# Kernel optimization log

Hardware: AMD Instinct MI355X
Metric: run time of the kernel (lower is better)

The kernel has to match this reference:

```python
import jax, jax.numpy as jnp
import numpy as np

B, D, C, K = 1024, 64, 100000, 5  # batch, feature dim, n_classes, positives per sample


def setup_inputs() -> dict:
    key = jax.random.key(0)
    k1, k2, k3 = jax.random.split(key, 3)
    x = jax.random.normal(k1, (B, D), dtype=jnp.float32)
    W = jax.random.normal(k2, (D, C), dtype=jnp.float32) * 0.02
    b = jnp.zeros((C,), dtype=jnp.float32)
    # K distinct positive class ids per sample (setdiff1d assume_unique requires distinct)
    base = jax.random.randint(k3, (B, 1), 0, C)
    labels = (base + jnp.arange(K, dtype=jnp.int64)[None, :]) % C
    return {"x": x, "labels": labels, "W": W, "b": b}


def reference(x, labels, W, b):
    # classifier: logits [B, C]
    logits = x @ W + b
    # Original loop: for each positive p of a sample, CE over [p] + negatives
    # (negatives = all classes except ALL positives of that sample), label 0:
    #   loss_p = -(l_p - log(exp(l_p) + sum_{c in negatives} exp(l_c)))
    # Vectorized via total expsum minus the positives' contribution.
    m = jnp.max(logits, axis=1, keepdims=True)                    # [B, 1]
    e = jnp.exp(logits - m)                                       # [B, C]
    total = jnp.sum(e, axis=1, keepdims=True)                     # [B, 1]
    pos_logits = jnp.take_along_axis(logits, labels, axis=1)      # [B, K]
    pos_e = jnp.exp(pos_logits - m)                               # [B, K]
    neg_sum = total - jnp.sum(pos_e, axis=1, keepdims=True)       # [B, 1]
    denom = pos_e + neg_sum                                       # [B, K]
    losses = -(pos_logits - m - jnp.log(denom))                   # [B, K]
    # sum over all (sample, positive) pairs / total number of positives
    return jnp.sum(losses) / losses.size
```

## Files before the change

kernel.cpp:

```cpp
#include <hip/hip_runtime.h>

constexpr int Bn = 1024;
constexpr int Dn = 64;
constexpr int Cn = 100000;
constexpr int Kn = 5;
constexpr float LOG2E = 1.44269504088896f;

typedef float f32x4  __attribute__((ext_vector_type(4)));
typedef short bf16x8 __attribute__((ext_vector_type(8)));

__device__ __forceinline__ unsigned short f32_to_bf16(float f) {
  union { float f; unsigned int u; } v; v.f = f;
  unsigned int r = v.u + 0x7FFFu + ((v.u >> 16) & 1u);
  return (unsigned short)(r >> 16);
}
__device__ __forceinline__ float bf16_to_f32(unsigned short u) {
  union { unsigned int i; float f; } v; v.i = ((unsigned int)u) << 16; return v.f;
}

constexpr int SPLITS = 125;
constexpr int CPS    = Cn / SPLITS;
constexpr int NCH    = CPS / 32;
constexpr int SGRPS  = 4;
constexpr int NBLK_W = (Cn + 63) / 64;
constexpr int GEMM_GRID = 512;

__global__ __launch_bounds__(256) void prep_kernel(
    const float* __restrict__ x, const float* __restrict__ W,
    unsigned short* __restrict__ xb, unsigned short* __restrict__ Wt,
    float* __restrict__ out)
{
  const int tid = threadIdx.x;
  const int b   = blockIdx.x;
  if (b == 0 && tid == 0) *out = 0.f;
  if (b < NBLK_W) {
    __shared__ unsigned short tile[64][71];
    const int c0   = b * 64;
    const int cIdx = tid & 63, dIdx = tid >> 6;
#pragma unroll
    for (int k = 0; k < 16; ++k) {
      const int d = dIdx * 16 + k;
      const int c = c0 + cIdx;
      const float v = (c < Cn) ? W[(size_t)d * Cn + c] : 0.f;
      tile[d][cIdx] = f32_to_bf16(v);
    }
    __syncthreads();
    const int cl = tid >> 2, dq = tid & 3;
    if (c0 + cl < Cn) {
      bf16x8 o0, o1;
#pragma unroll
      for (int k = 0; k < 8; ++k) o0[k] = (short)tile[dq * 16 + k][cl];
#pragma unroll
      for (int k = 0; k < 8; ++k) o1[k] = (short)tile[dq * 16 + 8 + k][cl];
      unsigned short* dst = Wt + (size_t)(c0 + cl) * 64 + dq * 16;
      *reinterpret_cast<bf16x8*>(dst)     = o0;
      *reinterpret_cast<bf16x8*>(dst + 8) = o1;
    }
  } else {
    const int i = ((b - NBLK_W) * 256 + tid) * 4;
    if (i < Bn * Dn) {
      const float4 v = *reinterpret_cast<const float4*>(x + i);
      ushort4 o;
      o.x = f32_to_bf16(v.x); o.y = f32_to_bf16(v.y);
      o.z = f32_to_bf16(v.z); o.w = f32_to_bf16(v.w);
      *reinterpret_cast<ushort4*>(xb + i) = o;
    }
  }
}

__device__ __forceinline__ void loadChunk(
    const unsigned short* __restrict__ Wt, const float* __restrict__ bias,
    int cb, int lr, int lg, bf16x8 (&b)[2][2], float (&bb)[2])
{
  const unsigned short* p0 = Wt + (size_t)(cb + lr) * 64 + lg * 8;
  const unsigned short* p1 = p0 + 16 * 64;
  b[0][0] = *reinterpret_cast<const bf16x8*>(p0);
  b[0][1] = *reinterpret_cast<const bf16x8*>(p0 + 32);
  b[1][0] = *reinterpret_cast<const bf16x8*>(p1);
  b[1][1] = *reinterpret_cast<const bf16x8*>(p1 + 32);
  bb[0] = bias[cb + lr] * LOG2E;
  bb[1] = bias[cb + 16 + lr] * LOG2E;
}

__device__ __forceinline__ void computeChunk(
    const bf16x8 (&a)[4][2], const bf16x8 (&b)[2][2], const float (&bb)[2],
    float (&esum)[4][4])
{
  f32x4 acc[4][2];
#pragma unroll
  for (int t = 0; t < 4; ++t) {
    acc[t][0] = f32x4{0.f, 0.f, 0.f, 0.f};
    acc[t][1] = f32x4{0.f, 0.f, 0.f, 0.f};
  }
#pragma unroll
  for (int t = 0; t < 4; ++t) {
    acc[t][0] = __builtin_amdgcn_mfma_f32_16x16x32_bf16(a[t][0], b[0][0], acc[t][0], 0, 0, 0);
    acc[t][1] = __builtin_amdgcn_mfma_f32_16x16x32_bf16(a[t][0], b[1][0], acc[t][1], 0, 0, 0);
    acc[t][0] = __builtin_amdgcn_mfma_f32_16x16x32_bf16(a[t][1], b[0][1], acc[t][0], 0, 0, 0);
    acc[t][1] = __builtin_amdgcn_mfma_f32_16x16x32_bf16(a[t][1], b[1][1], acc[t][1], 0, 0, 0);
  }
#pragma unroll
  for (int t = 0; t < 4; ++t)
#pragma unroll
    for (int j = 0; j < 4; ++j) {
      const float e0 = __builtin_amdgcn_exp2f(fmaf(acc[t][0][j], LOG2E, bb[0]));
      const float e1 = __builtin_amdgcn_exp2f(fmaf(acc[t][1][j], LOG2E, bb[1]));
      esum[t][j] += e0 + e1;
    }
}

__global__ __launch_bounds__(256) void gemm_expsum_kernel(
    const unsigned short* __restrict__ xb, const unsigned short* __restrict__ Wt,
    const float* __restrict__ bias, float* __restrict__ P)
{
  const int b    = blockIdx.x;
  const int xcd  = b & 7;
  const int slot = b >> 3;
  const int split = xcd * 16 + (slot >> 2);
  const int sgrp  = slot & 3;
  if (split >= SPLITS) return;

  const int tid  = threadIdx.x;
  const int lane = tid & 63, wid = tid >> 6;
  const int lr = lane & 15, lg = lane >> 4;
  const int sbase = sgrp * 256 + wid * 64;
  const int cb0   = split * CPS;

  bf16x8 a[4][2];
#pragma unroll
  for (int t = 0; t < 4; ++t) {
    const unsigned short* ap = xb + (size_t)(sbase + t * 16 + lr) * 64 + lg * 8;
    a[t][0] = *reinterpret_cast<const bf16x8*>(ap);
    a[t][1] = *reinterpret_cast<const bf16x8*>(ap + 32);
  }

  float esum[4][4];
#pragma unroll
  for (int t = 0; t < 4; ++t)
#pragma unroll
    for (int j = 0; j < 4; ++j) esum[t][j] = 0.f;

  bf16x8 bX[2][2]; float bbX[2];
  bf16x8 bY[2][2]; float bbY[2];
  loadChunk(Wt, bias, cb0, lr, lg, bX, bbX);
#pragma unroll 1
  for (int ch = 0; ch < NCH; ch += 2) {
    if (ch + 1 < NCH) loadChunk(Wt, bias, cb0 + (ch + 1) * 32, lr, lg, bY, bbY);
    computeChunk(a, bX, bbX, esum);
    if (ch + 1 < NCH) {
      if (ch + 2 < NCH) loadChunk(Wt, bias, cb0 + (ch + 2) * 32, lr, lg, bX, bbX);
      computeChunk(a, bY, bbY, esum);
    }
  }

  float red[4][4];
#pragma unroll
  for (int t = 0; t < 4; ++t)
#pragma unroll
    for (int j = 0; j < 4; ++j) {
      float v = esum[t][j];
      v += __shfl_xor(v, 1, 64);
      v += __shfl_xor(v, 2, 64);
      v += __shfl_xor(v, 4, 64);
      v += __shfl_xor(v, 8, 64);
      red[t][j] = v;
    }
  if (lr == 0) {
#pragma unroll
    for (int t = 0; t < 4; ++t)
#pragma unroll
      for (int j = 0; j < 4; ++j)
        P[(size_t)(sbase + t * 16 + lg * 4 + j) * SPLITS + split] = red[t][j];
  }
}

__global__ __launch_bounds__(64) void loss2_kernel(
    const unsigned short* __restrict__ xb, const int* __restrict__ labels,
    const unsigned short* __restrict__ Wt, const float* __restrict__ bias,
    const float* __restrict__ P, float* __restrict__ out)
{
  const int i = blockIdx.x, lane = threadIdx.x;
  float acc = P[(size_t)i * SPLITS + lane];
  if (lane + 64 < SPLITS) acc += P[(size_t)i * SPLITS + lane + 64];
#pragma unroll
  for (int off = 32; off > 0; off >>= 1) acc += __shfl_xor(acc, off, 64);
  const float Si = acc;

  const float xv = bf16_to_f32(xb[i * Dn + lane]);
  float l[Kn];
#pragma unroll
  for (int p = 0; p < Kn; ++p) {
    const int c = labels[i * Kn + p];
    float v = xv * bf16_to_f32(Wt[(size_t)c * 64 + lane]);
#pragma unroll
    for (int off = 32; off > 0; off >>= 1) v += __shfl_xor(v, off, 64);
    l[p] = v + bias[c];
  }
  if (lane == 0) {
    float Psum = 0.f;
#pragma unroll
    for (int p = 0; p < Kn; ++p) Psum += __expf(l[p]);
    const float neg = Si - Psum;
    float lsum = 0.f;
#pragma unroll
    for (int p = 0; p < Kn; ++p)
      lsum += __logf(__expf(l[p]) + neg) - l[p];
    atomicAdd(out, lsum * (1.0f / (float)(Bn * Kn)));
  }
}

constexpr int NB  = 128;
constexpr int NPB = (Cn + NB - 1) / NB;
constexpr int NPBpad = 784;

__global__ __launch_bounds__(256) void cvt_x_kernel(
    const float* __restrict__ x, unsigned short* __restrict__ xb)
{
  const int i = (blockIdx.x * 256 + threadIdx.x) * 4;
  const float4 v = *reinterpret_cast<const float4*>(x + i);
  ushort4 o;
  o.x = f32_to_bf16(v.x); o.y = f32_to_bf16(v.y);
  o.z = f32_to_bf16(v.z); o.w = f32_to_bf16(v.w);
  *reinterpret_cast<ushort4*>(xb + i) = o;
}

__global__ __launch_bounds__(256) void expsum_mfma_kernel(
    const unsigned short* __restrict__ xb, const float* __restrict__ W,
    const float* __restrict__ bias, float* __restrict__ P,
    float* __restrict__ S, int use_partials)
{
  __shared__ float S_lds[4][Bn];
  const int tid  = threadIdx.x;
  const int lane = tid & 63, wid = tid >> 6;
  const int lg = lane >> 4, lr = lane & 15;
  const int cbase = blockIdx.x * NB + wid * 32;

  for (int i = tid; i < 4 * Bn; i += 256) (&S_lds[0][0])[i] = 0.f;

  bf16x8 bfrag[2][2];
  float  bval[2];
#pragma unroll
  for (int t = 0; t < 2; ++t) {
    const int c  = cbase + t * 16 + lr;
    const bool ok = (c < Cn);
    bval[t] = ok ? bias[c] * LOG2E : -1e38f;
#pragma unroll
    for (int h = 0; h < 2; ++h) {
      bf16x8 bf;
#pragma unroll
      for (int j = 0; j < 8; ++j) {
        const int d = h * 32 + lg * 8 + j;
        const float w = ok ? W[(size_t)d * Cn + c] : 0.f;
        bf[j] = (short)f32_to_bf16(w);
      }
      bfrag[t][h] = bf;
    }
  }
  __syncthreads();

#pragma unroll 1
  for (int ch = 0; ch < Bn / 16; ++ch) {
    const int s = ch * 16 + lr;
    const bf16x8 a0 = *reinterpret_cast<const bf16x8*>(xb + (size_t)s * Dn + lg * 8);
    const bf16x8 a1 = *reinterpret_cast<const bf16x8*>(xb + (size_t)s * Dn + 32 + lg * 8);
    f32x4 acc0 = {0.f, 0.f, 0.f, 0.f};
    f32x4 acc1 = {0.f, 0.f, 0.f, 0.f};
    acc0 = __builtin_amdgcn_mfma_f32_16x16x32_bf16(a0, bfrag[0][0], acc0, 0, 0, 0);
    acc1 = __builtin_amdgcn_mfma_f32_16x16x32_bf16(a0, bfrag[1][0], acc1, 0, 0, 0);
    acc0 = __builtin_amdgcn_mfma_f32_16x16x32_bf16(a1, bfrag[0][1], acc0, 0, 0, 0);
    acc1 = __builtin_amdgcn_mfma_f32_16x16x32_bf16(a1, bfrag[1][1], acc1, 0, 0, 0);

    float v[4];
#pragma unroll
    for (int j = 0; j < 4; ++j) {
      const float e0 = __builtin_amdgcn_exp2f(fmaf(acc0[j], LOG2E, bval[0]));
      const float e1 = __builtin_amdgcn_exp2f(fmaf(acc1[j], LOG2E, bval[1]));
      v[j] = e0 + e1;
    }
#pragma unroll
    for (int j = 0; j < 4; ++j) {
      v[j] += __shfl_xor(v[j], 1, 64);
      v[j] += __shfl_xor(v[j], 2, 64);
      v[j] += __shfl_xor(v[j], 4, 64);
      v[j] += __shfl_xor(v[j], 8, 64);
    }
    if (lr == 0) {
#pragma unroll
      for (int j = 0; j < 4; ++j)
        S_lds[wid][ch * 16 + lg * 4 + j] += v[j];
    }
  }
  __syncthreads();

  if (use_partials) {
    for (int s2 = tid; s2 < Bn; s2 += 256) {
      const float v = S_lds[0][s2] + S_lds[1][s2] + S_lds[2][s2] + S_lds[3][s2];
      P[(size_t)s2 * NPBpad + blockIdx.x] = v;
    }
  } else {
    for (int s2 = tid; s2 < Bn; s2 += 256) {
      const float v = S_lds[0][s2] + S_lds[1][s2] + S_lds[2][s2] + S_lds[3][s2];
      atomicAdd(&S[s2], v);
    }
  }
}

__global__ __launch_bounds__(64) void loss_kernel(
    const float* __restrict__ x, const int* __restrict__ labels,
    const float* __restrict__ W, const float* __restrict__ bias,
    const float* __restrict__ P, const float* __restrict__ S,
    float* __restrict__ out, int use_partials)
{
  const int i    = blockIdx.x;
  const int lane = threadIdx.x;

  float Si;
  if (use_partials) {
    float acc = 0.f;
    for (int j = lane; j < NPB; j += 64) acc += P[(size_t)i * NPBpad + j];
#pragma unroll
    for (int off = 32; off > 0; off >>= 1) acc += __shfl_xor(acc, off, 64);
    Si = acc;
  } else {
    Si = S[i];
  }

  const float xv = x[i * Dn + lane];
  float l[Kn];
#pragma unroll
  for (int p = 0; p < Kn; ++p) {
    const int c = labels[i * Kn + p];
    float v = xv * W[(size_t)lane * Cn + c];
#pragma unroll
    for (int off = 32; off > 0; off >>= 1) v += __shfl_xor(v, off, 64);
    l[p] = v + bias[c];
  }

  if (lane == 0) {
    float Psum = 0.f;
#pragma unroll
    for (int p = 0; p < Kn; ++p) Psum += __expf(l[p]);
    const float neg = Si - Psum;
    float lsum = 0.f;
#pragma unroll
    for (int p = 0; p < Kn; ++p)
      lsum += __logf(__expf(l[p]) + neg) - l[p];
    atomicAdd(out, lsum * (1.0f / (float)(Bn * Kn)));
  }
}

extern "C" void kernel_launch(void* const* d_in, const int* in_sizes, int n_in,
                              void* d_out, int out_size, void* d_ws, size_t ws_size,
                              hipStream_t stream) {
  const float* x      = (const float*)d_in[0];
  const int*   labels = (const int*)d_in[1];
  const float* W      = (const float*)d_in[2];
  const float* bias   = (const float*)d_in[3];
  float*       out    = (float*)d_out;
  char*        ws     = (char*)d_ws;

  const size_t off_xb = 0;
  const size_t off_P  = (size_t)Bn * Dn * 2;
  const size_t off_Wt = off_P + (size_t)SPLITS * Bn * 4;
  const size_t need_new = off_Wt + (size_t)Cn * Dn * 2;

  if (ws_size >= need_new) {
    unsigned short* xb = (unsigned short*)(ws + off_xb);
    float*          P  = (float*)(ws + off_P);
    unsigned short* Wt = (unsigned short*)(ws + off_Wt);
    const int prep_blocks = NBLK_W + (Bn * Dn) / (256 * 4);
    prep_kernel<<<prep_blocks, 256, 0, stream>>>(x, W, xb, Wt, out);
    gemm_expsum_kernel<<<GEMM_GRID, 256, 0, stream>>>(xb, Wt, bias, P);
    loss2_kernel<<<Bn, 64, 0, stream>>>(xb, labels, Wt, bias, P, out);
    return;
  }

  hipMemsetAsync(out, 0, sizeof(float), stream);
  float*          Sg = (float*)ws;
  unsigned short* xb = (unsigned short*)(ws + 4096);
  float*          Pp = (float*)(ws + 4096 + (size_t)Bn * Dn * 2);
  const size_t need_old = 4096 + (size_t)Bn * Dn * 2 + (size_t)Bn * NPBpad * 4;
  const int use_partials = (ws_size >= need_old) ? 1 : 0;
  if (!use_partials) hipMemsetAsync(Sg, 0, Bn * sizeof(float), stream);

  cvt_x_kernel<<<(Bn * Dn) / (256 * 4), 256, 0, stream>>>(x, xb);
  expsum_mfma_kernel<<<NPB, 256, 0, stream>>>(xb, W, bias, Pp, Sg, use_partials);
  loss_kernel<<<Bn, 64, 0, stream>>>(x, labels, W, bias, Pp, Sg, out, use_partials);
}
```

Baseline: 60.74 us.

## Fuse W transpose/convert and x conversion into the GEMM expsum kernel

Removes the separate prep kernel: each GEMM block now converts and transposes its own 800-column slice of W into bf16 in the workspace, and converts x to bf16 in registers, pre-scaled by log2e. The bias is folded into the MFMA accumulator's initial value, which drops the per-element fma before exp2. This saves one launch and one round trip of x through memory. In exchange, each of the 4 row-group blocks sharing a split redundantly converts the same W slice with strided, poorly coalesced column reads. The slice must also be written and synced before the MFMA loop can start.

```diff
diff --git a/kernel.cpp b/kernel.cpp
--- a/kernel.cpp
+++ b/kernel.cpp
@@ -5,6 +5,7 @@
 constexpr int Cn = 100000;
 constexpr int Kn = 5;
 constexpr float LOG2E = 1.44269504088896f;
+constexpr float LN2   = 0.69314718055994531f;
 
 typedef float f32x4  __attribute__((ext_vector_type(4)));
 typedef short bf16x8 __attribute__((ext_vector_type(8)));
@@ -21,52 +22,7 @@
 constexpr int SPLITS = 125;
 constexpr int CPS    = Cn / SPLITS;
 constexpr int NCH    = CPS / 32;
-constexpr int SGRPS  = 4;
-constexpr int NBLK_W = (Cn + 63) / 64;
 constexpr int GEMM_GRID = 512;
-
-__global__ __launch_bounds__(256) void prep_kernel(
-    const float* __restrict__ x, const float* __restrict__ W,
-    unsigned short* __restrict__ xb, unsigned short* __restrict__ Wt,
-    float* __restrict__ out)
-{
-  const int tid = threadIdx.x;
-  const int b   = blockIdx.x;
-  if (b == 0 && tid == 0) *out = 0.f;
-  if (b < NBLK_W) {
-    __shared__ unsigned short tile[64][71];
-    const int c0   = b * 64;
-    const int cIdx = tid & 63, dIdx = tid >> 6;
-#pragma unroll
-    for (int k = 0; k < 16; ++k) {
-      const int d = dIdx * 16 + k;
-      const int c = c0 + cIdx;
-      const float v = (c < Cn) ? W[(size_t)d * Cn + c] : 0.f;
-      tile[d][cIdx] = f32_to_bf16(v);
-    }
-    __syncthreads();
-    const int cl = tid >> 2, dq = tid & 3;
-    if (c0 + cl < Cn) {
-      bf16x8 o0, o1;
-#pragma unroll
-      for (int k = 0; k < 8; ++k) o0[k] = (short)tile[dq * 16 + k][cl];
-#pragma unroll
-      for (int k = 0; k < 8; ++k) o1[k] = (short)tile[dq * 16 + 8 + k][cl];
-      unsigned short* dst = Wt + (size_t)(c0 + cl) * 64 + dq * 16;
-      *reinterpret_cast<bf16x8*>(dst)     = o0;
-      *reinterpret_cast<bf16x8*>(dst + 8) = o1;
-    }
-  } else {
-    const int i = ((b - NBLK_W) * 256 + tid) * 4;
-    if (i < Bn * Dn) {
-      const float4 v = *reinterpret_cast<const float4*>(x + i);
-      ushort4 o;
-      o.x = f32_to_bf16(v.x); o.y = f32_to_bf16(v.y);
-      o.z = f32_to_bf16(v.z); o.w = f32_to_bf16(v.w);
-      *reinterpret_cast<ushort4*>(xb + i) = o;
-    }
-  }
-}
 
 __device__ __forceinline__ void loadChunk(
     const unsigned short* __restrict__ Wt, const float* __restrict__ bias,
@@ -89,8 +45,8 @@
   f32x4 acc[4][2];
 #pragma unroll
   for (int t = 0; t < 4; ++t) {
-    acc[t][0] = f32x4{0.f, 0.f, 0.f, 0.f};
-    acc[t][1] = f32x4{0.f, 0.f, 0.f, 0.f};
+    acc[t][0] = f32x4{bb[0], bb[0], bb[0], bb[0]};
+    acc[t][1] = f32x4{bb[1], bb[1], bb[1], bb[1]};
   }
 #pragma unroll
   for (int t = 0; t < 4; ++t) {
@@ -103,15 +59,16 @@
   for (int t = 0; t < 4; ++t)
 #pragma unroll
     for (int j = 0; j < 4; ++j) {
-      const float e0 = __builtin_amdgcn_exp2f(fmaf(acc[t][0][j], LOG2E, bb[0]));
-      const float e1 = __builtin_amdgcn_exp2f(fmaf(acc[t][1][j], LOG2E, bb[1]));
+      const float e0 = __builtin_amdgcn_exp2f(acc[t][0][j]);
+      const float e1 = __builtin_amdgcn_exp2f(acc[t][1][j]);
       esum[t][j] += e0 + e1;
     }
 }
 
-__global__ __launch_bounds__(256) void gemm_expsum_kernel(
-    const unsigned short* __restrict__ xb, const unsigned short* __restrict__ Wt,
-    const float* __restrict__ bias, float* __restrict__ P)
+__global__ __launch_bounds__(256) void fused_gemm_kernel(
+    const float* __restrict__ x, const float* __restrict__ W,
+    const float* __restrict__ bias, unsigned short* __restrict__ Wt,
+    float* __restrict__ P, float* __restrict__ out)
 {
   const int b    = blockIdx.x;
   const int xcd  = b & 7;
@@ -121,6 +78,8 @@
   if (split >= SPLITS) return;
 
   const int tid  = threadIdx.x;
+  if (b == 0 && tid == 0) *out = 0.f;
+
   const int lane = tid & 63, wid = tid >> 6;
   const int lr = lane & 15, lg = lane >> 4;
   const int sbase = sgrp * 256 + wid * 64;
@@ -129,10 +88,44 @@
   bf16x8 a[4][2];
 #pragma unroll
   for (int t = 0; t < 4; ++t) {
-    const unsigned short* ap = xb + (size_t)(sbase + t * 16 + lr) * 64 + lg * 8;
-    a[t][0] = *reinterpret_cast<const bf16x8*>(ap);
-    a[t][1] = *reinterpret_cast<const bf16x8*>(ap + 32);
-  }
+    const float* xp = x + (size_t)(sbase + t * 16 + lr) * 64 + lg * 8;
+    const float4 v0 = *reinterpret_cast<const float4*>(xp);
+    const float4 v1 = *reinterpret_cast<const float4*>(xp + 4);
+    const float4 v2 = *reinterpret_cast<const float4*>(xp + 32);
+    const float4 v3 = *reinterpret_cast<const float4*>(xp + 36);
+    bf16x8 a0, a1;
+    a0[0] = (short)f32_to_bf16(v0.x * LOG2E);
+    a0[1] = (short)f32_to_bf16(v0.y * LOG2E);
+    a0[2] = (short)f32_to_bf16(v0.z * LOG2E);
+    a0[3] = (short)f32_to_bf16(v0.w * LOG2E);
+    a0[4] = (short)f32_to_bf16(v1.x * LOG2E);
+    a0[5] = (short)f32_to_bf16(v1.y * LOG2E);
+    a0[6] = (short)f32_to_bf16(v1.z * LOG2E);
+    a0[7] = (short)f32_to_bf16(v1.w * LOG2E);
+    a1[0] = (short)f32_to_bf16(v2.x * LOG2E);
+    a1[1] = (short)f32_to_bf16(v2.y * LOG2E);
+    a1[2] = (short)f32_to_bf16(v2.z * LOG2E);
+    a1[3] = (short)f32_to_bf16(v2.w * LOG2E);
+    a1[4] = (short)f32_to_bf16(v3.x * LOG2E);
+    a1[5] = (short)f32_to_bf16(v3.y * LOG2E);
+    a1[6] = (short)f32_to_bf16(v3.z * LOG2E);
+    a1[7] = (short)f32_to_bf16(v3.w * LOG2E);
+    a[t][0] = a0;
+    a[t][1] = a1;
+  }
+
+#pragma unroll 1
+  for (int k = 0; k < 25; ++k) {
+    const int u   = tid + k * 256;
+    const int oct = u & 7;
+    const int c   = u >> 3;
+    const float* wp = W + (size_t)(oct * 8) * Cn + (cb0 + c);
+    bf16x8 o;
+#pragma unroll
+    for (int j = 0; j < 8; ++j) o[j] = (short)f32_to_bf16(wp[(size_t)j * Cn]);
+    *reinterpret_cast<bf16x8*>(Wt + (size_t)(cb0 + c) * 64 + oct * 8) = o;
+  }
+  __syncthreads();
 
   float esum[4][4];
 #pragma unroll
@@ -175,7 +168,7 @@
 }
 
 __global__ __launch_bounds__(64) void loss2_kernel(
-    const unsigned short* __restrict__ xb, const int* __restrict__ labels,
+    const float* __restrict__ x, const int* __restrict__ labels,
     const unsigned short* __restrict__ Wt, const float* __restrict__ bias,
     const float* __restrict__ P, float* __restrict__ out)
 {
@@ -186,25 +179,25 @@
   for (int off = 32; off > 0; off >>= 1) acc += __shfl_xor(acc, off, 64);
   const float Si = acc;
 
-  const float xv = bf16_to_f32(xb[i * Dn + lane]);
-  float l[Kn];
+  const float xv = bf16_to_f32(f32_to_bf16(x[i * Dn + lane] * LOG2E));
+  float l2[Kn];
 #pragma unroll
   for (int p = 0; p < Kn; ++p) {
     const int c = labels[i * Kn + p];
     float v = xv * bf16_to_f32(Wt[(size_t)c * 64 + lane]);
 #pragma unroll
     for (int off = 32; off > 0; off >>= 1) v += __shfl_xor(v, off, 64);
-    l[p] = v + bias[c];
+    l2[p] = v + bias[c] * LOG2E;
   }
   if (lane == 0) {
     float Psum = 0.f;
 #pragma unroll
-    for (int p = 0; p < Kn; ++p) Psum += __expf(l[p]);
+    for (int p = 0; p < Kn; ++p) Psum += __builtin_amdgcn_exp2f(l2[p]);
     const float neg = Si - Psum;
     float lsum = 0.f;
 #pragma unroll
     for (int p = 0; p < Kn; ++p)
-      lsum += __logf(__expf(l[p]) + neg) - l[p];
+      lsum += __logf(__builtin_amdgcn_exp2f(l2[p]) + neg) - l2[p] * LN2;
     atomicAdd(out, lsum * (1.0f / (float)(Bn * Kn)));
   }
 }
@@ -359,19 +352,15 @@
   float*       out    = (float*)d_out;
   char*        ws     = (char*)d_ws;
 
-  const size_t off_xb = 0;
-  const size_t off_P  = (size_t)Bn * Dn * 2;
-  const size_t off_Wt = off_P + (size_t)SPLITS * Bn * 4;
+  const size_t off_P  = 0;
+  const size_t off_Wt = (size_t)SPLITS * Bn * 4;
   const size_t need_new = off_Wt + (size_t)Cn * Dn * 2;
 
   if (ws_size >= need_new) {
-    unsigned short* xb = (unsigned short*)(ws + off_xb);
     float*          P  = (float*)(ws + off_P);
     unsigned short* Wt = (unsigned short*)(ws + off_Wt);
-    const int prep_blocks = NBLK_W + (Bn * Dn) / (256 * 4);
-    prep_kernel<<<prep_blocks, 256, 0, stream>>>(x, W, xb, Wt, out);
-    gemm_expsum_kernel<<<GEMM_GRID, 256, 0, stream>>>(xb, Wt, bias, P);
-    loss2_kernel<<<Bn, 64, 0, stream>>>(xb, labels, Wt, bias, P, out);
+    fused_gemm_kernel<<<GEMM_GRID, 256, 0, stream>>>(x, W, bias, Wt, P, out);
+    loss2_kernel<<<Bn, 64, 0, stream>>>(x, labels, Wt, bias, P, out);
     return;
   }
 
```

After: 74.30 us. +22.3%, slower.

## Fold log2e into x and bias into MFMA accumulator; raise split count

Applied to the files above, without the earlier changes.

Pre-scales x by log2(e) when converting to bf16 and seeds the MFMA accumulators with the scaled bias, so the exp epilogue becomes a bare exp2 with no per-element FMA. The GEMM grid grows from 500 to 2500 workgroups (625 splits) with a new XCD-aware block mapping, giving more parallelism and finer load balance at the cost of a larger partial-sum buffer and a longer reduction loop in the loss kernel. The loss kernel is adjusted to work in the log2 domain. Rounding x*log2e to bf16 slightly changes numerics.

```diff
diff --git a/kernel.cpp b/kernel.cpp
--- a/kernel.cpp
+++ b/kernel.cpp
@@ -5,6 +5,7 @@
 constexpr int Cn = 100000;
 constexpr int Kn = 5;
 constexpr float LOG2E = 1.44269504088896f;
+constexpr float LN2   = 0.69314718055994531f;
 
 typedef float f32x4  __attribute__((ext_vector_type(4)));
 typedef short bf16x8 __attribute__((ext_vector_type(8)));
@@ -18,12 +19,11 @@
   union { unsigned int i; float f; } v; v.i = ((unsigned int)u) << 16; return v.f;
 }
 
-constexpr int SPLITS = 125;
+constexpr int SPLITS = 625;
 constexpr int CPS    = Cn / SPLITS;
 constexpr int NCH    = CPS / 32;
-constexpr int SGRPS  = 4;
+constexpr int GRID   = SPLITS * 4;
 constexpr int NBLK_W = (Cn + 63) / 64;
-constexpr int GEMM_GRID = 512;
 
 __global__ __launch_bounds__(256) void prep_kernel(
     const float* __restrict__ x, const float* __restrict__ W,
@@ -61,8 +61,8 @@
     if (i < Bn * Dn) {
       const float4 v = *reinterpret_cast<const float4*>(x + i);
       ushort4 o;
-      o.x = f32_to_bf16(v.x); o.y = f32_to_bf16(v.y);
-      o.z = f32_to_bf16(v.z); o.w = f32_to_bf16(v.w);
+      o.x = f32_to_bf16(v.x * LOG2E); o.y = f32_to_bf16(v.y * LOG2E);
+      o.z = f32_to_bf16(v.z * LOG2E); o.w = f32_to_bf16(v.w * LOG2E);
       *reinterpret_cast<ushort4*>(xb + i) = o;
     }
   }
@@ -89,8 +89,8 @@
   f32x4 acc[4][2];
 #pragma unroll
   for (int t = 0; t < 4; ++t) {
-    acc[t][0] = f32x4{0.f, 0.f, 0.f, 0.f};
-    acc[t][1] = f32x4{0.f, 0.f, 0.f, 0.f};
+    acc[t][0] = f32x4{bb[0], bb[0], bb[0], bb[0]};
+    acc[t][1] = f32x4{bb[1], bb[1], bb[1], bb[1]};
   }
 #pragma unroll
   for (int t = 0; t < 4; ++t) {
@@ -103,8 +103,8 @@
   for (int t = 0; t < 4; ++t)
 #pragma unroll
     for (int j = 0; j < 4; ++j) {
-      const float e0 = __builtin_amdgcn_exp2f(fmaf(acc[t][0][j], LOG2E, bb[0]));
-      const float e1 = __builtin_amdgcn_exp2f(fmaf(acc[t][1][j], LOG2E, bb[1]));
+      const float e0 = __builtin_amdgcn_exp2f(acc[t][0][j]);
+      const float e1 = __builtin_amdgcn_exp2f(acc[t][1][j]);
       esum[t][j] += e0 + e1;
     }
 }
@@ -113,12 +113,10 @@
     const unsigned short* __restrict__ xb, const unsigned short* __restrict__ Wt,
     const float* __restrict__ bias, float* __restrict__ P)
 {
-  const int b    = blockIdx.x;
-  const int xcd  = b & 7;
-  const int slot = b >> 3;
-  const int split = xcd * 16 + (slot >> 2);
-  const int sgrp  = slot & 3;
-  if (split >= SPLITS) return;
+  const int b   = blockIdx.x;
+  const int xcd = b & 7, bs = b >> 3;
+  const int wgid = (xcd < 4 ? xcd * 313 : 1252 + (xcd - 4) * 312) + bs;
+  const int split = wgid >> 2, sgrp = wgid & 3;
 
   const int tid  = threadIdx.x;
   const int lane = tid & 63, wid = tid >> 6;
@@ -180,31 +178,31 @@
     const float* __restrict__ P, float* __restrict__ out)
 {
   const int i = blockIdx.x, lane = threadIdx.x;
-  float acc = P[(size_t)i * SPLITS + lane];
-  if (lane + 64 < SPLITS) acc += P[(size_t)i * SPLITS + lane + 64];
+  float acc = 0.f;
+  for (int j = lane; j < SPLITS; j += 64) acc += P[(size_t)i * SPLITS + j];
 #pragma unroll
   for (int off = 32; off > 0; off >>= 1) acc += __shfl_xor(acc, off, 64);
   const float Si = acc;
 
   const float xv = bf16_to_f32(xb[i * Dn + lane]);
-  float l[Kn];
+  float l2[Kn];
 #pragma unroll
   for (int p = 0; p < Kn; ++p) {
     const int c = labels[i * Kn + p];
     float v = xv * bf16_to_f32(Wt[(size_t)c * 64 + lane]);
 #pragma unroll
     for (int off = 32; off > 0; off >>= 1) v += __shfl_xor(v, off, 64);
-    l[p] = v + bias[c];
+    l2[p] = v + bias[c] * LOG2E;
   }
   if (lane == 0) {
     float Psum = 0.f;
 #pragma unroll
-    for (int p = 0; p < Kn; ++p) Psum += __expf(l[p]);
+    for (int p = 0; p < Kn; ++p) Psum += __builtin_amdgcn_exp2f(l2[p]);
     const float neg = Si - Psum;
     float lsum = 0.f;
 #pragma unroll
     for (int p = 0; p < Kn; ++p)
-      lsum += __logf(__expf(l[p]) + neg) - l[p];
+      lsum += __logf(__builtin_amdgcn_exp2f(l2[p]) + neg) - l2[p] * LN2;
     atomicAdd(out, lsum * (1.0f / (float)(Bn * Kn)));
   }
 }
@@ -370,7 +368,7 @@
     unsigned short* Wt = (unsigned short*)(ws + off_Wt);
     const int prep_blocks = NBLK_W + (Bn * Dn) / (256 * 4);
     prep_kernel<<<prep_blocks, 256, 0, stream>>>(x, W, xb, Wt, out);
-    gemm_expsum_kernel<<<GEMM_GRID, 256, 0, stream>>>(xb, Wt, bias, P);
+    gemm_expsum_kernel<<<GRID, 256, 0, stream>>>(xb, Wt, bias, P);
     loss2_kernel<<<Bn, 64, 0, stream>>>(xb, labels, Wt, bias, P, out);
     return;
   }
```

Result: slower. 70.85 us (+16.6%).
